# Kernel tuning notes

Measured on AMD Instinct MI355X. Metric: run time of the kernel, lower is better.

The kernel has to match this reference:

```python
import jax, jax.numpy as jnp
import numpy as np

EPS = 1e-5


def setup_inputs() -> dict:
    key = jax.random.key(0)
    ks = jax.random.split(key, 7)
    N, M, D, H, DM = 8192, 128, 64, 8, 1024  # tokens, num_memories, d_memory, heads, d_model
    return {
        "query": jax.random.normal(ks[0], (N, DM), dtype=jnp.float32),
        "addresses": jax.random.normal(ks[1], (M, D), dtype=jnp.float32),
        "memories": jax.random.normal(ks[2], (N, M, D), dtype=jnp.float32),
        "Wq": jax.random.normal(ks[3], (DM, H * D), dtype=jnp.float32) / np.sqrt(DM),
        "bq": jax.random.normal(ks[4], (H * D,), dtype=jnp.float32) * 0.01,
        "Wo": jax.random.normal(ks[5], (H * D, DM), dtype=jnp.float32) / np.sqrt(H * D),
        "bo": jax.random.normal(ks[6], (DM,), dtype=jnp.float32) * 0.01,
    }


def reference(query, addresses, memories, Wq, bq, Wo, bo):
    N = query.shape[0]
    M, D = addresses.shape
    # Query projection -> heads: (N, H, D)
    q = (query @ Wq + bq).reshape(N, -1, D)
    q = jax.nn.relu(q)  # kernel feature map on query
    # Keys: memory content + learned addresses, kernel feature map
    k = jax.nn.relu(memories + addresses)  # (N, M, D)
    # make_kernel: contract over the num_memories dim
    matrix = jnp.einsum("nmd,nme->nde", k, memories)  # (N, D, D)
    normalizer = jnp.sum(k, axis=-2)  # (N, D)
    # read_from_kernel
    numerator = jnp.einsum("nhd,nde->nhe", q, matrix)  # (N, H, D)
    denominator = jnp.einsum("nhd,nd->nh", q, normalizer)[..., None] + EPS
    attn = numerator / denominator  # (N, H, D)
    # merge heads back to d_model
    return attn.reshape(N, -1) @ Wo + bo
```

## Files before the change

kernel.cpp:

```cpp
#include <hip/hip_runtime.h>

typedef __bf16 bf16x8 __attribute__((ext_vector_type(8)));
typedef __bf16 bf16x4 __attribute__((ext_vector_type(4)));
typedef __bf16 bf16x2 __attribute__((ext_vector_type(2)));
typedef float  f32x4  __attribute__((ext_vector_type(4)));

__device__ __forceinline__ void gload_lds16(const void* g, void* l) {
    auto gp = reinterpret_cast<const __attribute__((address_space(1))) unsigned int*>(
        reinterpret_cast<uintptr_t>(g));
    auto lp = reinterpret_cast<__attribute__((address_space(3))) unsigned int*>(
        reinterpret_cast<uintptr_t>(l));
    __builtin_amdgcn_global_load_lds(gp, lp, 16, 0, 0);
}

__device__ __forceinline__ void xcd_remap(int lin, int& bx, int& by) {
    const int wgid = (lin & 7) * 64 + (lin >> 3);
    bx = wgid & 7;
    by = wgid >> 3;
}

__global__ __launch_bounds__(256) void prep_all(
    const float* __restrict__ Wq, const float* __restrict__ Wo,
    const float* __restrict__ adr,
    __bf16* __restrict__ WqT, __bf16* __restrict__ WoT,
    __bf16* __restrict__ adrb)
{
    __shared__ float tile[32][33];
    const int bid = blockIdx.x, tid = threadIdx.x;

    if (bid < 1024) {
        const float* src; __bf16* dst; int R, C, r0, c0;
        if (bid < 512) {
            src = Wq; dst = WqT; R = 1024; C = 512;
            c0 = (bid & 15) * 32; r0 = (bid >> 4) * 32;
        } else {
            const int b = bid - 512;
            src = Wo; dst = WoT; R = 512; C = 1024;
            c0 = (b & 31) * 32; r0 = (b >> 5) * 32;
        }
        const int tx = tid & 31, ty = tid >> 5;
        #pragma unroll
        for (int i = ty; i < 32; i += 8)
            tile[i][tx] = src[(size_t)(r0 + i) * C + c0 + tx];
        __syncthreads();
        #pragma unroll
        for (int i = ty; i < 32; i += 8)
            dst[(size_t)(c0 + i) * R + r0 + tx] = (__bf16)tile[tx][i];
    } else {
        const int i = (bid - 1024) * 256 + tid;
        f32x4 a = ((const f32x4*)adr)[2 * i];
        f32x4 b = ((const f32x4*)adr)[2 * i + 1];
        bf16x8 o;
        #pragma unroll
        for (int j = 0; j < 4; ++j) { o[j] = (__bf16)a[j]; o[4 + j] = (__bf16)b[j]; }
        ((bf16x8*)adrb)[i] = o;
    }
}

__global__ __launch_bounds__(256) void gemm_qproj(
    const float* __restrict__ A, const __bf16* __restrict__ BT,
    const float* __restrict__ bias, __bf16* __restrict__ Out,
    int M, int N, int K)
{
    __shared__ __bf16 As[2][128][40];
    __shared__ __bf16 Bs[2][64][32];

    const int tid = threadIdx.x, lane = tid & 63, w = tid >> 6;
    const int wm = w >> 1, wn = w & 1;
    int bx, by;
    xcd_remap(blockIdx.x + 8 * blockIdx.y, bx, by);
    const int m0 = by * 128, n0 = bx * 64;
    const int r = lane & 15, g = lane >> 4;

    const int arow = tid >> 3, ac4 = (tid & 7) * 4;
    const float*  gA = A  + (size_t)(m0 + arow) * K + ac4;
    const __bf16* gB = BT + (size_t)(n0 + 16 * w + (lane >> 2)) * K + (lane & 3) * 8;

    f32x4 acc[4][2];
    const f32x4 zero = {0.f, 0.f, 0.f, 0.f};
    #pragma unroll
    for (int mi = 0; mi < 4; ++mi)
        #pragma unroll
        for (int ni = 0; ni < 2; ++ni) acc[mi][ni] = zero;

    const int NT = K / 32;

    {
        f32x4 la[4];
        #pragma unroll
        for (int i = 0; i < 4; ++i)
            la[i] = *(const f32x4*)(gA + (size_t)(32 * i) * K);
        gload_lds16(gB, &Bs[0][16 * w][0]);
        #pragma unroll
        for (int i = 0; i < 4; ++i) {
            bf16x4 b;
            #pragma unroll
            for (int j = 0; j < 4; ++j) b[j] = (__bf16)la[i][j];
            *(bf16x4*)&As[0][arow + 32 * i][ac4] = b;
        }
        __syncthreads();
    }

    int cur = 0;
    for (int t = 0; t < NT; ++t) {
        const int k0 = t * 32;
        f32x4 ln[4];
        if (t + 1 < NT) {
            #pragma unroll
            for (int i = 0; i < 4; ++i)
                ln[i] = *(const f32x4*)(gA + (size_t)(32 * i) * K + k0 + 32);
            gload_lds16(gB + k0 + 32, &Bs[cur ^ 1][16 * w][0]);
        }
        bf16x8 af[4], bfr[2];
        #pragma unroll
        for (int mi = 0; mi < 4; ++mi)
            af[mi] = *(const bf16x8*)&As[cur][wm * 64 + mi * 16 + r][g * 8];
        #pragma unroll
        for (int ni = 0; ni < 2; ++ni)
            bfr[ni] = *(const bf16x8*)&Bs[cur][wn * 32 + ni * 16 + r][g * 8];
        #pragma unroll
        for (int mi = 0; mi < 4; ++mi)
            #pragma unroll
            for (int ni = 0; ni < 2; ++ni)
                acc[mi][ni] = __builtin_amdgcn_mfma_f32_16x16x32_bf16(
                    af[mi], bfr[ni], acc[mi][ni], 0, 0, 0);
        if (t + 1 < NT) {
            #pragma unroll
            for (int i = 0; i < 4; ++i) {
                bf16x4 b;
                #pragma unroll
                for (int j = 0; j < 4; ++j) b[j] = (__bf16)ln[i][j];
                *(bf16x4*)&As[cur ^ 1][arow + 32 * i][ac4] = b;
            }
        }
        __syncthreads();
        cur ^= 1;
    }

    const int orow = m0 + wm * 64 + g * 4;
    const int ocol = n0 + wn * 32 + r;
    #pragma unroll
    for (int ni = 0; ni < 2; ++ni) {
        const float bb = bias[ocol + ni * 16];
        #pragma unroll
        for (int mi = 0; mi < 4; ++mi) {
            #pragma unroll
            for (int q = 0; q < 4; ++q) {
                float v = fmaxf(acc[mi][ni][q] + bb, 0.f);
                Out[(size_t)(orow + mi * 16 + q) * N + ocol + ni * 16] = (__bf16)v;
            }
        }
    }
}

__global__ __launch_bounds__(256) void gemm_oproj(
    const __bf16* __restrict__ A, const __bf16* __restrict__ BT,
    const float* __restrict__ bias, float* __restrict__ Out,
    int M, int N, int K)
{
    __shared__ __bf16 As[2][128][32];
    __shared__ __bf16 Bs[2][128][32];

    const int tid = threadIdx.x, lane = tid & 63, w = tid >> 6;
    const int wm = w >> 1, wn = w & 1;
    int bx, by;
    xcd_remap(blockIdx.x + 8 * blockIdx.y, bx, by);
    const int m0 = by * 128, n0 = bx * 128;
    const int r = lane & 15, g = lane >> 4;

    const int srow = lane >> 2;
    const int scol = (lane & 3) * 8;
    const __bf16* gA = A  + (size_t)(m0 + 32 * w + srow) * K + scol;
    const __bf16* gB = BT + (size_t)(n0 + 32 * w + srow) * K + scol;

    f32x4 acc[4][4];
    const f32x4 zero = {0.f, 0.f, 0.f, 0.f};
    #pragma unroll
    for (int mi = 0; mi < 4; ++mi)
        #pragma unroll
        for (int ni = 0; ni < 4; ++ni) acc[mi][ni] = zero;

    const int NT = K / 32;

    gload_lds16(gA,          &As[0][32 * w][0]);
    gload_lds16(gA + 16 * K, &As[0][32 * w + 16][0]);
    gload_lds16(gB,          &Bs[0][32 * w][0]);
    gload_lds16(gB + 16 * K, &Bs[0][32 * w + 16][0]);
    __syncthreads();

    int cur = 0;
    for (int t = 0; t < NT; ++t) {
        const int k0 = t * 32;
        if (t + 1 < NT) {
            gload_lds16(gA + k0 + 32,          &As[cur ^ 1][32 * w][0]);
            gload_lds16(gA + 16 * K + k0 + 32, &As[cur ^ 1][32 * w + 16][0]);
            gload_lds16(gB + k0 + 32,          &Bs[cur ^ 1][32 * w][0]);
            gload_lds16(gB + 16 * K + k0 + 32, &Bs[cur ^ 1][32 * w + 16][0]);
        }
        bf16x8 af[4], bfr[4];
        #pragma unroll
        for (int mi = 0; mi < 4; ++mi)
            af[mi] = *(const bf16x8*)&As[cur][wm * 64 + mi * 16 + r][g * 8];
        #pragma unroll
        for (int ni = 0; ni < 4; ++ni)
            bfr[ni] = *(const bf16x8*)&Bs[cur][wn * 64 + ni * 16 + r][g * 8];
        #pragma unroll
        for (int mi = 0; mi < 4; ++mi)
            #pragma unroll
            for (int ni = 0; ni < 4; ++ni)
                acc[mi][ni] = __builtin_amdgcn_mfma_f32_16x16x32_bf16(
                    af[mi], bfr[ni], acc[mi][ni], 0, 0, 0);
        __syncthreads();
        cur ^= 1;
    }

    const int orow = m0 + wm * 64 + g * 4;
    const int ocol = n0 + wn * 64 + r;
    #pragma unroll
    for (int ni = 0; ni < 4; ++ni) {
        const float bb = bias[ocol + ni * 16];
        #pragma unroll
        for (int mi = 0; mi < 4; ++mi) {
            #pragma unroll
            for (int q = 0; q < 4; ++q) {
                Out[(size_t)(orow + mi * 16 + q) * N + ocol + ni * 16]
                    = acc[mi][ni][q] + bb;
            }
        }
    }
}

__device__ __forceinline__ int kbyte(int m, int e) {
    return m * 128 + ((((e >> 3) ^ (m & 7))) << 4) + (e & 7) * 2;
}

__global__ void memory_attn_mfma(
    const __bf16* __restrict__ Q,
    const float*  __restrict__ mem,
    const __bf16* __restrict__ adrb,
    __bf16* __restrict__ attn)
{
    __shared__ __align__(16) unsigned char kbuf[4][4096];
    __shared__ __align__(16) unsigned char tbuf[4][5120];
    __shared__ float denl[4][8];

    const int tid = threadIdx.x, lane = tid & 63, w = tid >> 6;
    const int n = blockIdx.x * 4 + w;
    const int v = lane & 15, g = lane >> 4;

    unsigned char* kb = kbuf[w];
    unsigned char* tb = tbuf[w];

    const __bf16* qp = Q + (size_t)n * 512 + v * 64 + 8 * g;
    const bf16x8 qf0 = *(const bf16x8*)(qp);
    const bf16x8 qf1 = *(const bf16x8*)(qp + 32);

    f32x4 acc[4];
    const f32x4 zero = {0.f, 0.f, 0.f, 0.f};
    #pragma unroll
    for (int nb = 0; nb < 4; ++nb) acc[nb] = zero;
    float psum = 0.f;

    for (int c = 0; c < 4; ++c) {
        const int mb = c * 32;
        #pragma unroll
        for (int i = 0; i < 4; ++i) {
            const int mo = 8 * i + 2 * g;
            const int e  = 4 * v;
            const float* pm = mem + (((size_t)n * 128 + mb + mo) * 64 + e);
            const f32x4 m0 = *(const f32x4*)pm;
            const f32x4 m1 = *(const f32x4*)(pm + 64);
            const bf16x4 a0 = *(const bf16x4*)(adrb + (size_t)(mb + mo) * 64 + e);
            const bf16x4 a1 = *(const bf16x4*)(adrb + (size_t)(mb + mo + 1) * 64 + e);
            bf16x4 k0, k1;
            #pragma unroll
            for (int j = 0; j < 4; ++j) {
                k0[j] = (__bf16)fmaxf(m0[j] + (float)a0[j], 0.f);
                k1[j] = (__bf16)fmaxf(m1[j] + (float)a1[j], 0.f);
            }
            *(bf16x4*)(kb + kbyte(mo,     e)) = k0;
            *(bf16x4*)(kb + kbyte(mo + 1, e)) = k1;
            const int kap = 8 * ((mo >> 2) & 3) + 4 * (mo >> 4) + (mo & 3);
            #pragma unroll
            for (int j2 = 0; j2 < 4; ++j2) {
                bf16x2 p = { (__bf16)m0[j2], (__bf16)m1[j2] };
                *(bf16x2*)(tb + (size_t)(e + j2) * 80 + kap * 2) = p;
            }
        }

        f32x4 sA0 = zero, sA1 = zero;
        {
            const bf16x8 a00 = *(const bf16x8*)(kb + kbyte(v,      8 * g));
            const bf16x8 a01 = *(const bf16x8*)(kb + kbyte(v,      32 + 8 * g));
            const bf16x8 a10 = *(const bf16x8*)(kb + kbyte(v + 16, 8 * g));
            const bf16x8 a11 = *(const bf16x8*)(kb + kbyte(v + 16, 32 + 8 * g));
            sA0 = __builtin_amdgcn_mfma_f32_16x16x32_bf16(a00, qf0, sA0, 0, 0, 0);
            sA0 = __builtin_amdgcn_mfma_f32_16x16x32_bf16(a01, qf1, sA0, 0, 0, 0);
            sA1 = __builtin_amdgcn_mfma_f32_16x16x32_bf16(a10, qf0, sA1, 0, 0, 0);
            sA1 = __builtin_amdgcn_mfma_f32_16x16x32_bf16(a11, qf1, sA1, 0, 0, 0);
        }
        psum += sA0[0] + sA0[1] + sA0[2] + sA0[3]
              + sA1[0] + sA1[1] + sA1[2] + sA1[3];

        bf16x8 pa;
        #pragma unroll
        for (int q = 0; q < 4; ++q) {
            pa[q]     = (__bf16)sA0[q];
            pa[4 + q] = (__bf16)sA1[q];
        }

        #pragma unroll
        for (int nb = 0; nb < 4; ++nb) {
            const bf16x8 bf = *(const bf16x8*)(tb + (size_t)(16 * nb + v) * 80 + 16 * g);
            acc[nb] = __builtin_amdgcn_mfma_f32_16x16x32_bf16(pa, bf, acc[nb], 0, 0, 0);
        }
    }

    psum += __shfl_xor(psum, 16);
    psum += __shfl_xor(psum, 32);
    if (lane < 8) denl[w][lane] = psum;

    if (g < 2) {
        const f32x4 d4 = *(const f32x4*)&denl[w][4 * g];
        float inv[4];
        #pragma unroll
        for (int q = 0; q < 4; ++q) inv[q] = 1.f / (d4[q] + 1e-5f);
        #pragma unroll
        for (int nb = 0; nb < 4; ++nb) {
            #pragma unroll
            for (int q = 0; q < 4; ++q) {
                attn[(size_t)n * 512 + (4 * g + q) * 64 + 16 * nb + v] =
                    (__bf16)(acc[nb][q] * inv[q]);
            }
        }
    }
}

extern "C" void kernel_launch(void* const* d_in, const int* in_sizes, int n_in,
                              void* d_out, int out_size, void* d_ws, size_t ws_size,
                              hipStream_t stream)
{
    const float* query     = (const float*)d_in[0];
    const float* addresses = (const float*)d_in[1];
    const float* memories  = (const float*)d_in[2];
    const float* Wq        = (const float*)d_in[3];
    const float* bq        = (const float*)d_in[4];
    const float* Wo        = (const float*)d_in[5];
    const float* bo        = (const float*)d_in[6];
    float* out = (float*)d_out;

    char* ws = (char*)d_ws;
    __bf16* WqT  = (__bf16*)(ws);
    __bf16* WoT  = (__bf16*)(ws + (1 << 20));
    __bf16* Qb   = (__bf16*)(ws + (2 << 20));
    __bf16* Ab   = (__bf16*)(ws + (10 << 20));
    __bf16* Adrb = (__bf16*)(ws + (18 << 20));

    prep_all<<<1028, 256, 0, stream>>>(Wq, Wo, addresses, WqT, WoT, Adrb);

    gemm_qproj<<<dim3(512 / 64, 8192 / 128), 256, 0, stream>>>(
        query, WqT, bq, Qb, 8192, 512, 1024);

    memory_attn_mfma<<<dim3(8192 / 4), 256, 0, stream>>>(Qb, memories, Adrb, Ab);

    gemm_oproj<<<dim3(1024 / 128, 8192 / 128), 256, 0, stream>>>(
        Ab, WoT, bo, out, 8192, 1024, 512);
}
```

Measured before the change: 115.4 us.

## Triple-buffer o-proj GEMM with 512 threads and partial vmcnt barriers

Result: no change. 115.5 us (+0.1%).

```diff
diff --git a/kernel.cpp b/kernel.cpp
--- a/kernel.cpp
+++ b/kernel.cpp
@@ -11,6 +11,19 @@
     auto lp = reinterpret_cast<__attribute__((address_space(3))) unsigned int*>(
         reinterpret_cast<uintptr_t>(l));
     __builtin_amdgcn_global_load_lds(gp, lp, 16, 0, 0);
+}
+
+__device__ __forceinline__ void barrier_vm2_lgkm() {
+    __builtin_amdgcn_sched_barrier(0);
+    asm volatile("s_waitcnt vmcnt(2) lgkmcnt(0)" ::: "memory");
+    __builtin_amdgcn_s_barrier();
+    __builtin_amdgcn_sched_barrier(0);
+}
+__device__ __forceinline__ void barrier_vm0_lgkm() {
+    __builtin_amdgcn_sched_barrier(0);
+    asm volatile("s_waitcnt vmcnt(0) lgkmcnt(0)" ::: "memory");
+    __builtin_amdgcn_s_barrier();
+    __builtin_amdgcn_sched_barrier(0);
 }
 
 __device__ __forceinline__ void xcd_remap(int lin, int& bx, int& by) {
@@ -153,13 +166,13 @@
     }
 }
 
-__global__ __launch_bounds__(256) void gemm_oproj(
+__global__ __launch_bounds__(512) void gemm_oproj(
     const __bf16* __restrict__ A, const __bf16* __restrict__ BT,
     const float* __restrict__ bias, float* __restrict__ Out,
     int M, int N, int K)
 {
-    __shared__ __bf16 As[2][128][32];
-    __shared__ __bf16 Bs[2][128][32];
+    __shared__ __bf16 As[3][128][32];
+    __shared__ __bf16 Bs[3][128][32];
 
     const int tid = threadIdx.x, lane = tid & 63, w = tid >> 6;
     const int wm = w >> 1, wn = w & 1;
@@ -170,57 +183,61 @@
 
     const int srow = lane >> 2;
     const int scol = (lane & 3) * 8;
-    const __bf16* gA = A  + (size_t)(m0 + 32 * w + srow) * K + scol;
-    const __bf16* gB = BT + (size_t)(n0 + 32 * w + srow) * K + scol;
-
-    f32x4 acc[4][4];
+    const __bf16* gA = A  + (size_t)(m0 + 16 * w + srow) * K + scol;
+    const __bf16* gB = BT + (size_t)(n0 + 16 * w + srow) * K + scol;
+
+    f32x4 acc[2][4];
     const f32x4 zero = {0.f, 0.f, 0.f, 0.f};
     #pragma unroll
-    for (int mi = 0; mi < 4; ++mi)
+    for (int mi = 0; mi < 2; ++mi)
         #pragma unroll
         for (int ni = 0; ni < 4; ++ni) acc[mi][ni] = zero;
 
     const int NT = K / 32;
 
-    gload_lds16(gA,          &As[0][32 * w][0]);
-    gload_lds16(gA + 16 * K, &As[0][32 * w + 16][0]);
-    gload_lds16(gB,          &Bs[0][32 * w][0]);
-    gload_lds16(gB + 16 * K, &Bs[0][32 * w + 16][0]);
-    __syncthreads();
-
-    int cur = 0;
+    gload_lds16(gA,      &As[0][16 * w][0]);
+    gload_lds16(gB,      &Bs[0][16 * w][0]);
+    gload_lds16(gA + 32, &As[1][16 * w][0]);
+    gload_lds16(gB + 32, &Bs[1][16 * w][0]);
+    __builtin_amdgcn_sched_barrier(0);
+    asm volatile("s_waitcnt vmcnt(2)" ::: "memory");
+    __builtin_amdgcn_s_barrier();
+    __builtin_amdgcn_sched_barrier(0);
+
+    int buf = 0;
     for (int t = 0; t < NT; ++t) {
-        const int k0 = t * 32;
-        if (t + 1 < NT) {
-            gload_lds16(gA + k0 + 32,          &As[cur ^ 1][32 * w][0]);
-            gload_lds16(gA + 16 * K + k0 + 32, &As[cur ^ 1][32 * w + 16][0]);
-            gload_lds16(gB + k0 + 32,          &Bs[cur ^ 1][32 * w][0]);
-            gload_lds16(gB + 16 * K + k0 + 32, &Bs[cur ^ 1][32 * w + 16][0]);
-        }
-        bf16x8 af[4], bfr[4];
-        #pragma unroll
-        for (int mi = 0; mi < 4; ++mi)
-            af[mi] = *(const bf16x8*)&As[cur][wm * 64 + mi * 16 + r][g * 8];
+        if (t + 2 < NT) {
+            const int nb = (buf + 2 >= 3) ? buf - 1 : buf + 2;
+            gload_lds16(gA + (t + 2) * 32, &As[nb][16 * w][0]);
+            gload_lds16(gB + (t + 2) * 32, &Bs[nb][16 * w][0]);
+        }
+        bf16x8 af[2], bfr[4];
+        #pragma unroll
+        for (int mi = 0; mi < 2; ++mi)
+            af[mi] = *(const bf16x8*)&As[buf][wm * 32 + mi * 16 + r][g * 8];
         #pragma unroll
         for (int ni = 0; ni < 4; ++ni)
-            bfr[ni] = *(const bf16x8*)&Bs[cur][wn * 64 + ni * 16 + r][g * 8];
-        #pragma unroll
-        for (int mi = 0; mi < 4; ++mi)
+            bfr[ni] = *(const bf16x8*)&Bs[buf][wn * 64 + ni * 16 + r][g * 8];
+        #pragma unroll
+        for (int mi = 0; mi < 2; ++mi)
             #pragma unroll
             for (int ni = 0; ni < 4; ++ni)
                 acc[mi][ni] = __builtin_amdgcn_mfma_f32_16x16x32_bf16(
                     af[mi], bfr[ni], acc[mi][ni], 0, 0, 0);
-        __syncthreads();
-        cur ^= 1;
-    }
-
-    const int orow = m0 + wm * 64 + g * 4;
+        if (t + 1 < NT) {
+            if (t + 2 < NT) barrier_vm2_lgkm();
+            else            barrier_vm0_lgkm();
+        }
+        buf = (buf + 1 >= 3) ? 0 : buf + 1;
+    }
+
+    const int orow = m0 + wm * 32 + g * 4;
     const int ocol = n0 + wn * 64 + r;
     #pragma unroll
     for (int ni = 0; ni < 4; ++ni) {
         const float bb = bias[ocol + ni * 16];
         #pragma unroll
-        for (int mi = 0; mi < 4; ++mi) {
+        for (int mi = 0; mi < 2; ++mi) {
             #pragma unroll
             for (int q = 0; q < 4; ++q) {
                 Out[(size_t)(orow + mi * 16 + q) * N + ocol + ni * 16]
@@ -363,6 +380,6 @@
 
     memory_attn_mfma<<<dim3(8192 / 4), 256, 0, stream>>>(Qb, memories, Adrb, Ab);
 
-    gemm_oproj<<<dim3(1024 / 128, 8192 / 128), 256, 0, stream>>>(
+    gemm_oproj<<<dim3(1024 / 128, 8192 / 128), 512, 0, stream>>>(
         Ab, WoT, bo, out, 8192, 1024, 512);
 }
```
